# Kernel tuning notes

Hardware: AMD Instinct MI355X
Metric: run time of the kernel (lower is better)

## Reference

```python
import jax, jax.numpy as jnp
import numpy as np

B, S, D_MODEL, HEAD, D_KV = 8, 1024, 1024, 16, 64


def setup_inputs() -> dict:
    key = jax.random.key(0)
    ks = jax.random.split(key, 10)
    std = 1.0 / np.sqrt(D_MODEL)
    inp = {
        "queries": jax.random.normal(ks[0], (B, S, D_MODEL), jnp.float32),
        "keys": jax.random.normal(ks[1], (B, S, D_MODEL), jnp.float32),
        "values": jax.random.normal(ks[2], (B, S, D_MODEL), jnp.float32),
        "group_prob": jax.random.uniform(ks[3], (B, 1, S, S), jnp.float32),
        "attention_mask": jax.random.randint(ks[4], (B, 1, S, S), 0, 2, jnp.int32),
        "Wq": jax.random.normal(ks[5], (HEAD * D_KV, D_MODEL), jnp.float32) * std,
        "bq": jnp.zeros((HEAD * D_KV,), jnp.float32),
        "Wk": jax.random.normal(ks[6], (HEAD * D_KV, D_MODEL), jnp.float32) * std,
        "bk": jnp.zeros((HEAD * D_KV,), jnp.float32),
        "Wv": jax.random.normal(ks[7], (HEAD * D_KV, D_MODEL), jnp.float32) * std,
        "bv": jnp.zeros((HEAD * D_KV,), jnp.float32),
    }
    return inp


def reference(queries, keys, values, group_prob, attention_mask, Wq, bq, Wk, bk, Wv, bv):
    b, nq = queries.shape[:2]
    # QKV projections -> [b, head, seq, d_kv]
    q = (queries @ Wq.T + bq).reshape(b, nq, HEAD, D_KV).transpose(0, 2, 1, 3)
    k = (keys @ Wk.T + bk).reshape(b, -1, HEAD, D_KV).transpose(0, 2, 1, 3)
    v = (values @ Wv.T + bv).reshape(b, -1, HEAD, D_KV).transpose(0, 2, 1, 3)
    # scaled scores [b, head, nq, nk]
    att = jnp.einsum("bhqd,bhkd->bhqk", q, k) / np.sqrt(D_KV).astype(np.float32)
    # NOTE: the original torch code calls att.masked_fill(...) (out-of-place)
    # and discards the result, so attention_mask has no effect. Replicated here.
    att = jax.nn.softmax(att, axis=-1)
    att = att * group_prob  # post-softmax group scaling (breaks fused SDPA)
    out = jnp.einsum("bhqk,bhkd->bhqd", att, v)
    return out.transpose(0, 2, 1, 3).reshape(b, nq, HEAD * D_KV)
```

## Files before the change

### kernel.cpp

```cpp
#include <hip/hip_runtime.h>

#define B_SZ 8
#define S_SZ 1024
#define DM   1024
#define NH   16
#define DK   64

typedef __bf16 bf16;
typedef __bf16 bf16x8 __attribute__((ext_vector_type(8)));
typedef float  f32x4  __attribute__((ext_vector_type(4)));

__device__ __forceinline__ f32x4 mfma16x16x32(bf16x8 a, bf16x8 b, f32x4 c) {
    return __builtin_amdgcn_mfma_f32_16x16x32_bf16(a, b, c, 0, 0, 0);
}

typedef const __attribute__((address_space(1))) void* gptr_t;
typedef __attribute__((address_space(3))) void*       sptr_t;
__device__ __forceinline__ void async_cp16(const void* g, void* s) {
    __builtin_amdgcn_global_load_lds((gptr_t)g, (sptr_t)s, 16, 0, 0);
}

__global__ __launch_bounds__(256)
void cvt_kernel(const float* __restrict__ x0, const float* __restrict__ x1,
                const float* __restrict__ x2, const float* __restrict__ w0,
                const float* __restrict__ w1, const float* __restrict__ w2,
                bf16* __restrict__ xb, bf16* __restrict__ wb)
{
    const int z = blockIdx.y;
    const float* src;
    bf16* dst;
    int n;
    if (z < 3) {
        src = (z == 0) ? x0 : (z == 1) ? x1 : x2;
        dst = xb + (size_t)z * (8u * 1024 * 1024);
        n = 8 * 1024 * 1024;
    } else {
        const int w = z - 3;
        src = (w == 0) ? w0 : (w == 1) ? w1 : w2;
        dst = wb + (size_t)w * (1024 * 1024);
        n = 1024 * 1024;
    }
    const int idx = (blockIdx.x * 256 + threadIdx.x) * 8;
    if (idx >= n) return;
    const float4 a = *(const float4*)(src + idx);
    const float4 c = *(const float4*)(src + idx + 4);
    union { bf16 h[8]; uint4 u; } pk;
    pk.h[0] = (bf16)a.x; pk.h[1] = (bf16)a.y; pk.h[2] = (bf16)a.z; pk.h[3] = (bf16)a.w;
    pk.h[4] = (bf16)c.x; pk.h[5] = (bf16)c.y; pk.h[6] = (bf16)c.z; pk.h[7] = (bf16)c.w;
    *(uint4*)(dst + idx) = pk.u;
}

__global__ __launch_bounds__(256)
void cvt_gp_kernel(const float* __restrict__ gp, bf16* __restrict__ gpb)
{
    const int idx = (blockIdx.x * 256 + threadIdx.x) * 8;
    const float4 a = *(const float4*)(gp + idx);
    const float4 c = *(const float4*)(gp + idx + 4);
    union { bf16 h[8]; uint4 u; } pk;
    pk.h[0] = (bf16)a.x; pk.h[1] = (bf16)a.y; pk.h[2] = (bf16)a.z; pk.h[3] = (bf16)a.w;
    pk.h[4] = (bf16)c.x; pk.h[5] = (bf16)c.y; pk.h[6] = (bf16)c.z; pk.h[7] = (bf16)c.w;
    *(uint4*)(gpb + idx) = pk.u;
}

__global__ __launch_bounds__(256, 2)
void qkv_gemm(const bf16* __restrict__ xb, const bf16* __restrict__ wb,
              const float* __restrict__ bq, const float* __restrict__ bk,
              const float* __restrict__ bv,
              bf16* __restrict__ qb, bf16* __restrict__ kb,
              bf16* __restrict__ vb)
{
    const int z = blockIdx.z;
    const bf16* A  = xb + (size_t)z * (8u * 1024 * 1024);
    const bf16* Bm = wb + (size_t)z * (1024 * 1024);
    const float* bias = (z == 0) ? bq : (z == 1) ? bk : bv;

    __shared__ bf16 Ash[128 * 64];
    __shared__ bf16 Bsh[128 * 64];

    const int tid  = threadIdx.x;
    const int wid  = tid >> 6;
    const int lane = tid & 63;
    const int quad = lane >> 4;
    const int l16  = lane & 15;
    const int wm   = wid >> 1, wn = wid & 1;
    const int bm   = blockIdx.x, bn = blockIdx.y;

    f32x4 acc[4][4] = {};

    for (int k0 = 0; k0 < DM; k0 += 64) {
        __syncthreads();
        #pragma unroll
        for (int i = 0; i < 4; ++i) {
            const int e   = (i * 256 + tid) * 8;
            const int row = e >> 6;
            const int c   = ((e >> 3) & 7) ^ (row & 7);
            async_cp16(A  + (size_t)(bm * 128 + row) * DM + k0 + c * 8, &Ash[e]);
            async_cp16(Bm + (size_t)(bn * 128 + row) * DM + k0 + c * 8, &Bsh[e]);
        }
        __syncthreads();

        #pragma unroll
        for (int ks = 0; ks < 2; ++ks) {
            bf16x8 af[4], bfr[4];
            #pragma unroll
            for (int mi = 0; mi < 4; ++mi) {
                const int row = wm * 64 + mi * 16 + l16;
                af[mi] = *(const bf16x8*)&Ash[row * 64 + (((ks * 4 + quad) ^ (l16 & 7)) << 3)];
            }
            #pragma unroll
            for (int ni = 0; ni < 4; ++ni) {
                const int row = wn * 64 + ni * 16 + l16;
                bfr[ni] = *(const bf16x8*)&Bsh[row * 64 + (((ks * 4 + quad) ^ (l16 & 7)) << 3)];
            }
            #pragma unroll
            for (int mi = 0; mi < 4; ++mi)
                #pragma unroll
                for (int ni = 0; ni < 4; ++ni)
                    acc[mi][ni] = mfma16x16x32(af[mi], bfr[ni], acc[mi][ni]);
        }
    }

    #pragma unroll
    for (int ni = 0; ni < 4; ++ni) {
        const int n    = bn * 128 + wn * 64 + ni * 16 + l16;
        const float bv_ = bias[n];
        const int h = n >> 6, d = n & 63;
        #pragma unroll
        for (int mi = 0; mi < 4; ++mi) {
            const int m0 = bm * 128 + wm * 64 + mi * 16 + quad * 4;
            const int b  = m0 >> 10;
            const int s0 = m0 & 1023;
            if (z == 2) {
                union { bf16 h4[4]; uint2 u; } pk;
                #pragma unroll
                for (int r = 0; r < 4; ++r) pk.h4[r] = (bf16)(acc[mi][ni][r] + bv_);
                *(uint2*)(vb + ((size_t)((b * NH + h) * DK + d)) * S_SZ + s0) = pk.u;
            } else {
                bf16* dst      = (z == 0) ? qb : kb;
                const float sc = (z == 0) ? 0.125f : 1.0f;
                #pragma unroll
                for (int r = 0; r < 4; ++r)
                    dst[((size_t)(b * NH + h) * S_SZ + (s0 + r)) * DK + d] =
                        (bf16)((acc[mi][ni][r] + bv_) * sc);
            }
        }
    }
}

__global__ __launch_bounds__(512, 6)
void attn_kernel(const bf16* __restrict__ qb, const bf16* __restrict__ kb,
                 const bf16* __restrict__ vb, const bf16* __restrict__ gpb,
                 float* __restrict__ out)
{
    __shared__ bf16 Ksh[2][64 * 64];
    __shared__ bf16 Vsh[2][64 * 64];
    __shared__ bf16 Psh[8][16 * 72];
    __shared__ float Lsh[8][16];

    const int tid  = threadIdx.x;
    const int wid  = tid >> 6;
    const int lane = tid & 63;
    const int quad = lane >> 4;
    const int l16  = lane & 15;

    const int lid = blockIdx.x + (int)gridDim.x * blockIdx.y;
    const int b   = lid & 7;
    const int h   = (lid >> 3) & (NH - 1);
    const int qt  = lid >> 7;
    const int bh  = b * NH + h;
    const int q0  = qt * 128 + wid * 16;

    const bf16* qr = qb + ((size_t)bh * S_SZ + q0 + l16) * DK;
    const bf16x8 qf0 = *(const bf16x8*)(qr + quad * 8);
    const bf16x8 qf1 = *(const bf16x8*)(qr + 32 + quad * 8);

    f32x4 acc[4] = {};
    float lpart = 0.0f;

    const bf16* gpq = gpb + ((size_t)b * S_SZ + q0 + l16) * S_SZ;
    const bf16* kbh = kb + (size_t)bh * (S_SZ * DK);
    const bf16* vbh = vb + (size_t)bh * ((size_t)DK * S_SZ);

    auto STAGE = [&](int t, int bufi) {
        const int e   = tid * 8;
        const int row = e >> 6;
        const int c   = ((e >> 3) & 7) ^ (row & 7);
        async_cp16(kbh + (size_t)(t * 64 + row) * DK + c * 8, &Ksh[bufi][e]);
        async_cp16(vbh + (size_t)row * S_SZ + t * 64 + c * 8, &Vsh[bufi][e]);
    };
    auto GPLOAD = [&](int t, ushort4 (&g)[4]) {
        #pragma unroll
        for (int nb = 0; nb < 4; ++nb)
            g[nb] = *(const ushort4*)(gpq + t * 64 + nb * 16 + quad * 4);
    };
    auto COMPUTE = [&](const bf16* Kb, const bf16* Vb, const ushort4 (&g)[4]) {
        f32x4 sc[4];
        #pragma unroll
        for (int nb = 0; nb < 4; ++nb) {
            const int row = nb * 16 + l16;
            const bf16x8 kf0 = *(const bf16x8*)&Kb[row * 64 + ((quad ^ (l16 & 7)) << 3)];
            const bf16x8 kf1 = *(const bf16x8*)&Kb[row * 64 + (((4 + quad) ^ (l16 & 7)) << 3)];
            f32x4 s = {0.0f, 0.0f, 0.0f, 0.0f};
            s = mfma16x16x32(kf0, qf0, s);
            s = mfma16x16x32(kf1, qf1, s);
            sc[nb] = s;
        }
        #pragma unroll
        for (int nb = 0; nb < 4; ++nb) {
            union { bf16 h4[4]; uint2 u; } pk;
            const unsigned short* gu = (const unsigned short*)&g[nb];
            #pragma unroll
            for (int r = 0; r < 4; ++r) {
                const float pv = __expf(sc[nb][r]);
                lpart += pv;
                const float gg = __uint_as_float(((unsigned)gu[r]) << 16);
                pk.h4[r] = (bf16)(pv * gg);
            }
            *(uint2*)&Psh[wid][l16 * 72 + nb * 16 + quad * 4] = pk.u;
        }
        bf16x8 pf[2];
        #pragma unroll
        for (int j = 0; j < 2; ++j)
            pf[j] = *(const bf16x8*)&Psh[wid][l16 * 72 + j * 32 + quad * 8];
        #pragma unroll
        for (int ni = 0; ni < 4; ++ni) {
            const int vrow = ni * 16 + l16;
            #pragma unroll
            for (int j = 0; j < 2; ++j) {
                const bf16x8 vf =
                    *(const bf16x8*)&Vb[vrow * 64 + (((j * 4 + quad) ^ (l16 & 7)) << 3)];
                acc[ni] = mfma16x16x32(pf[j], vf, acc[ni]);
            }
        }
    };

    ushort4 gplA[4], gplB[4];
    STAGE(0, 0);
    GPLOAD(0, gplA);
    __syncthreads();

    for (int tt = 0; tt < 8; ++tt) {
        const int t0 = tt * 2;
        STAGE(t0 + 1, 1);
        GPLOAD(t0 + 1, gplB);
        COMPUTE(Ksh[0], Vsh[0], gplA);
        __syncthreads();
        if (t0 + 2 < 16) {
            STAGE(t0 + 2, 0);
            GPLOAD(t0 + 2, gplA);
        }
        COMPUTE(Ksh[1], Vsh[1], gplB);
        __syncthreads();
    }

    lpart += __shfl_xor(lpart, 16, 64);
    lpart += __shfl_xor(lpart, 32, 64);
    if (quad == 0) Lsh[wid][l16] = 1.0f / lpart;
    __syncthreads();

    #pragma unroll
    for (int r = 0; r < 4; ++r) {
        const float inv = Lsh[wid][quad * 4 + r];
        float* orow = out + ((size_t)b * S_SZ + q0 + quad * 4 + r) * DM + h * DK;
        #pragma unroll
        for (int ni = 0; ni < 4; ++ni)
            orow[ni * 16 + l16] = acc[ni][r] * inv;
    }
}

extern "C" void kernel_launch(void* const* d_in, const int* in_sizes, int n_in,
                              void* d_out, int out_size, void* d_ws, size_t ws_size,
                              hipStream_t stream) {
    const float* queries = (const float*)d_in[0];
    const float* keys    = (const float*)d_in[1];
    const float* values  = (const float*)d_in[2];
    const float* gp      = (const float*)d_in[3];
    const float* Wq = (const float*)d_in[5];
    const float* bq = (const float*)d_in[6];
    const float* Wk = (const float*)d_in[7];
    const float* bk = (const float*)d_in[8];
    const float* Wv = (const float*)d_in[9];
    const float* bv = (const float*)d_in[10];
    float* out = (float*)d_out;

    bf16* xb = (bf16*)d_ws;
    bf16* wb = xb + (size_t)3 * 8 * 1024 * 1024;
    bf16* qb = wb + (size_t)3 * 1024 * 1024;
    bf16* kb = qb + (size_t)B_SZ * NH * S_SZ * DK;
    bf16* vb = kb + (size_t)B_SZ * NH * S_SZ * DK;
    bf16* gpb = xb;
    (void)ws_size; (void)in_sizes; (void)n_in; (void)out_size;

    dim3 gc(4096, 6);
    cvt_kernel<<<gc, 256, 0, stream>>>(queries, keys, values, Wq, Wk, Wv, xb, wb);

    dim3 g1(64, 8, 3);
    qkv_gemm<<<g1, 256, 0, stream>>>(xb, wb, bq, bk, bv, qb, kb, vb);

    cvt_gp_kernel<<<dim3(4096), 256, 0, stream>>>(gp, gpb);

    dim3 g2(B_SZ * NH , S_SZ / 128 , 1);
    attn_kernel<<<g2, 512, 0, stream>>>(qb, kb, vb, gpb, out);
}
```

Baseline: 332.5 us.

## Triple-buffer K/V tiles with explicit vmcnt waits and raw barriers

Replaces the double-buffered K/V LDS pipeline with a three-stage ring, issuing async global-to-LDS copies two tiles ahead. It uses explicit s_waitcnt vmcnt counts and raw s_barrier calls in place of __syncthreads, so later loads can stay in flight while the current tile is computed. The loop is fully unrolled through a macro. This raises LDS use per block, which can lower occupancy, and the hand-counted vmcnt values must match the number of outstanding loads exactly or the kernel will read stale data.

Result: no change. 337.7 us (+1.5%).

```diff
diff --git a/kernel.cpp b/kernel.cpp
--- a/kernel.cpp
+++ b/kernel.cpp
@@ -18,6 +18,17 @@
 typedef __attribute__((address_space(3))) void*       sptr_t;
 __device__ __forceinline__ void async_cp16(const void* g, void* s) {
     __builtin_amdgcn_global_load_lds((gptr_t)g, (sptr_t)s, 16, 0, 0);
+}
+
+template<int N> __device__ __forceinline__ void wait_vmcnt() {
+    asm volatile("s_waitcnt vmcnt(%0)" :: "n"(N) : "memory");
+}
+__device__ __forceinline__ void block_barrier() {
+    __builtin_amdgcn_sched_barrier(0);
+    asm volatile("" ::: "memory");
+    __builtin_amdgcn_s_barrier();
+    asm volatile("" ::: "memory");
+    __builtin_amdgcn_sched_barrier(0);
 }
 
 __global__ __launch_bounds__(256)
@@ -152,8 +163,8 @@
                  const bf16* __restrict__ vb, const bf16* __restrict__ gpb,
                  float* __restrict__ out)
 {
-    __shared__ bf16 Ksh[2][64 * 64];
-    __shared__ bf16 Vsh[2][64 * 64];
+    __shared__ bf16 Ksh[3][64 * 64];
+    __shared__ bf16 Vsh[3][64 * 64];
     __shared__ bf16 Psh[8][16 * 72];
     __shared__ float Lsh[8][16];
 
@@ -234,24 +245,30 @@
         }
     };
 
-    ushort4 gplA[4], gplB[4];
+    ushort4 gpl[2][4];
+
     STAGE(0, 0);
-    GPLOAD(0, gplA);
-    __syncthreads();
-
-    for (int tt = 0; tt < 8; ++tt) {
-        const int t0 = tt * 2;
-        STAGE(t0 + 1, 1);
-        GPLOAD(t0 + 1, gplB);
-        COMPUTE(Ksh[0], Vsh[0], gplA);
-        __syncthreads();
-        if (t0 + 2 < 16) {
-            STAGE(t0 + 2, 0);
-            GPLOAD(t0 + 2, gplA);
-        }
-        COMPUTE(Ksh[1], Vsh[1], gplB);
-        __syncthreads();
-    }
+    STAGE(1, 1);
+    STAGE(2, 2);
+    GPLOAD(0, gpl[0]);
+    wait_vmcnt<8>();
+    block_barrier();
+
+#define KN(T) (4 + ((T)+2 < 16 ? 2 : 0) + ((T)+1 < 16 ? 4 : 0) + ((T)+3 < 16 ? 2 : 0))
+#define STEP(T) do {                                                      \
+        if ((T) + 1 < 16) GPLOAD((T) + 1, gpl[((T) + 1) & 1]);            \
+        COMPUTE(Ksh[(T) % 3], Vsh[(T) % 3], gpl[(T) & 1]);                \
+        block_barrier();               \
+        if ((T) + 3 < 16) STAGE((T) + 3, (T) % 3);                        \
+        if ((T) < 15) { wait_vmcnt<KN(T)>(); block_barrier(); }           \
+    } while (0)
+
+    STEP(0);  STEP(1);  STEP(2);  STEP(3);
+    STEP(4);  STEP(5);  STEP(6);  STEP(7);
+    STEP(8);  STEP(9);  STEP(10); STEP(11);
+    STEP(12); STEP(13); STEP(14); STEP(15);
+#undef STEP
+#undef KN
 
     lpart += __shfl_xor(lpart, 16, 64);
     lpart += __shfl_xor(lpart, 32, 64);
```
